# Performance work log

Measured on AMD Instinct MI355X. Metric: run time of the kernel, lower is better.

## Reference

```python
import jax, jax.numpy as jnp
import numpy as np

DIMS, K_SIZE, V_SIZE = 256, 64, 64
B, T = 4, 4096


def setup_inputs() -> dict:
    key = jax.random.key(0)
    k1, k2, k3, k4 = jax.random.split(key, 4)
    # glorot-uniform-style init for the projection weights
    def glorot(k, fan_in, fan_out):
        lim = jnp.sqrt(6.0 / (fan_in + fan_out))
        return jax.random.uniform(k, (fan_in, fan_out), jnp.float32, -lim, lim)
    return {
        "inputs": jax.random.normal(k1, (B, T, DIMS), jnp.float32),
        "key_w": glorot(k2, DIMS, K_SIZE),
        "query_w": glorot(k3, DIMS, K_SIZE),
        "value_w": glorot(k4, DIMS, V_SIZE),
    }


def reference(inputs, key_w, query_w, value_w):
    # QKV projections: [B,T,D] @ [D,k] -> [B,T,k]
    keys = jnp.einsum('btd,dk->btk', inputs, key_w)
    queries = jnp.einsum('btd,dk->btk', inputs, query_w)
    values = jnp.einsum('btd,dv->btv', inputs, value_w)
    # full causal score matrix [B,T,T] (faithful to explicit triu mask)
    logits = jnp.einsum('bqk,bsk->bqs', queries, keys)
    q_idx = jnp.arange(logits.shape[1])[:, None]
    s_idx = jnp.arange(logits.shape[2])[None, :]
    causal = s_idx <= q_idx  # lower-triangular incl. diagonal
    sqrt_k = jnp.sqrt(jnp.asarray(key_w.shape[1], jnp.float32))
    masked = jnp.where(causal[None], logits, -jnp.inf)
    probs = jax.nn.softmax(masked / sqrt_k, axis=2)
    read = jnp.einsum('bqs,bsv->bqv', probs, values)
    return jnp.concatenate([inputs, read], axis=-1)  # [B,T,D+V]
```

## Files before the change

### kernel.cpp

```cpp
#include <hip/hip_runtime.h>

#define DIMS 256
#define HK 64
#define NB 4
#define NT 4096
#define BT (NB * NT)
#define SMAX 8

typedef unsigned short u16;
typedef unsigned int u32;

using f32x4  = __attribute__((ext_vector_type(4))) float;
using bf16x8 = __attribute__((ext_vector_type(8))) short;
using u32x2  = __attribute__((ext_vector_type(2))) u32;

__device__ __forceinline__ u16 f2bf(float f) {
    u32 u = __float_as_uint(f);
    u = (u + 0x7FFFu + ((u >> 16) & 1u)) >> 16;
    return (u16)u;
}
__device__ __forceinline__ u32 pack2(float a, float b) {
    return (u32)f2bf(a) | ((u32)f2bf(b) << 16);
}
__device__ __forceinline__ float bf2f(short h) {
    return __uint_as_float(((u32)(u16)h) << 16);
}
__device__ __forceinline__ bf16x8 ldb8(const u16* p) {
    return *reinterpret_cast<const bf16x8*>(p);
}

__global__ __launch_bounds__(256) void prep_kernel(
    const float* __restrict__ x, const float* __restrict__ wk,
    const float* __restrict__ wq, const float* __restrict__ wv,
    float* __restrict__ out, u32* __restrict__ xb2, u16* __restrict__ Wt)
{
    const int stride = (int)(gridDim.x * blockDim.x);
    const int idx = (int)(blockIdx.x * blockDim.x + threadIdx.x);
    const f32x4* x4 = reinterpret_cast<const f32x4*>(x);
    f32x4* out4 = reinterpret_cast<f32x4*>(out);
    u32x2* xbv = reinterpret_cast<u32x2*>(xb2);

    for (int i = idx; i < BT * 64; i += stride) {
        f32x4 v = x4[i];
        out4[(size_t)(i >> 6) * 80 + (i & 63)] = v;
        u32x2 w;
        w.x = pack2(v[0], v[1]);
        w.y = pack2(v[2], v[3]);
        xbv[i] = w;
    }
    for (int i = idx; i < 12288; i += stride) {
        const int e0 = i * 4;
        const int m = e0 >> 14;
        const int r = e0 & 16383;
        const int col = r >> 8;
        const int k = r & 255;
        const float* w = (m == 0) ? wk : (m == 1) ? wq : wv;
        u32 w0 = pack2(w[(k + 0) * HK + col], w[(k + 1) * HK + col]);
        u32 w1 = pack2(w[(k + 2) * HK + col], w[(k + 3) * HK + col]);
        u32* p = reinterpret_cast<u32*>(Wt + e0);
        p[0] = w0; p[1] = w1;
    }
}

__global__ __launch_bounds__(64) void proj_kernel(
    const u16* __restrict__ xb, const u16* __restrict__ Wt,
    u16* __restrict__ Qb, u16* __restrict__ Kb, u16* __restrict__ Vt)
{
    const int l = (int)threadIdx.x;
    const int lo = l & 15;
    const int g = l >> 4;
    const int bid = (int)blockIdx.x;
    const int m = bid % 3;
    const int q0 = (bid / 3) * 16;

    bf16x8 a[8];
    const u16* xrow = xb + (size_t)(q0 + lo) * DIMS + g * 8;
    #pragma unroll
    for (int kf = 0; kf < 8; ++kf) a[kf] = ldb8(xrow + kf * 32);

    const u16* wb = Wt + m * (HK * DIMS);
    f32x4 acc[4];
    #pragma unroll
    for (int c = 0; c < 4; ++c) acc[c] = f32x4{0.f, 0.f, 0.f, 0.f};

    __builtin_amdgcn_s_setprio(1);
    #pragma unroll
    for (int c = 0; c < 4; ++c) {
        #pragma unroll
        for (int kf = 0; kf < 8; ++kf) {
            bf16x8 bf = ldb8(wb + (size_t)(16 * c + lo) * DIMS + kf * 32 + g * 8);
            acc[c] = __builtin_amdgcn_mfma_f32_16x16x32_bf16(a[kf], bf, acc[c], 0, 0, 0);
        }
    }
    __builtin_amdgcn_s_setprio(0);

    if (m == 2) {
        #pragma unroll
        for (int c = 0; c < 4; ++c)
            #pragma unroll
            for (int ii = 0; ii < 4; ++ii) {
                const int grow = q0 + 4 * g + ii;
                Vt[(size_t)((grow >> 12) * HK + 16 * c + lo) * NT + (grow & (NT - 1))] =
                    f2bf(acc[c][ii]);
            }
    } else {
        const float sc = (m == 1) ? 0.125f * 1.44269504f : 1.0f;
        u16* dst = (m == 1) ? Qb : Kb;
        #pragma unroll
        for (int c = 0; c < 4; ++c)
            #pragma unroll
            for (int ii = 0; ii < 4; ++ii)
                dst[(size_t)(q0 + 4 * g + ii) * HK + 16 * c + lo] = f2bf(acc[c][ii] * sc);
    }
}

template<bool MASK>
__device__ __forceinline__ void qk_tile(
    const u16* __restrict__ Kb_b, int s0, int colbase,
    const bf16x8 (&qf)[2][2], float (&pls)[2][4],
    u16 (&Pl)[32 * 72], int lo, int g, int q0)
{
    bf16x8 kk[2][2];
    #pragma unroll
    for (int kh = 0; kh < 2; ++kh)
        #pragma unroll
        for (int kf = 0; kf < 2; ++kf)
            kk[kh][kf] = ldb8(Kb_b + (size_t)(s0 + 16 * kh + lo) * HK + kf * 32 + g * 8);

    const f32x4 zz = f32x4{0.f, 0.f, 0.f, 0.f};
    f32x4 sv[2][2];
    __builtin_amdgcn_s_setprio(1);
    #pragma unroll
    for (int rh = 0; rh < 2; ++rh)
        #pragma unroll
        for (int kh = 0; kh < 2; ++kh) {
            sv[rh][kh] = __builtin_amdgcn_mfma_f32_16x16x32_bf16(qf[rh][0], kk[kh][0], zz, 0, 0, 0);
            sv[rh][kh] = __builtin_amdgcn_mfma_f32_16x16x32_bf16(qf[rh][1], kk[kh][1], sv[rh][kh], 0, 0, 0);
        }
    __builtin_amdgcn_s_setprio(0);

    #pragma unroll
    for (int rh = 0; rh < 2; ++rh)
        #pragma unroll
        for (int kh = 0; kh < 2; ++kh)
            #pragma unroll
            for (int ii = 0; ii < 4; ++ii) {
                float v = sv[rh][kh][ii];
                if (MASK) {
                    if (s0 + 16 * kh + lo > q0 + 16 * rh + 4 * g + ii) v = -1e30f;
                }
                const float p = __builtin_amdgcn_exp2f(v - 28.0f);
                pls[rh][ii] += p;
                Pl[(16 * rh + 4 * g + ii) * 72 + colbase + 16 * kh + lo] = f2bf(p);
            }
}

template<int NKF, bool MASK>
__device__ __forceinline__ void body(
    const u16* __restrict__ Kb_b, const u16* __restrict__ Vb, int s0,
    const bf16x8 (&qf)[2][2], float (&pls)[2][4], f32x4 (&o)[2][4],
    u16 (&Pl)[32 * 72], int lo, int g, int q0)
{
    bf16x8 vf[NKF][4];
    #pragma unroll
    for (int kf = 0; kf < NKF; ++kf)
        #pragma unroll
        for (int c = 0; c < 4; ++c)
            vf[kf][c] = ldb8(Vb + (size_t)(16 * c + lo) * NT + s0 + kf * 32 + g * 8);

    qk_tile<MASK>(Kb_b, s0, 0, qf, pls, Pl, lo, g, q0);
    if (NKF == 2) qk_tile<false>(Kb_b, s0 + 32, 32, qf, pls, Pl, lo, g, q0);

    bf16x8 pa[2][NKF];
    #pragma unroll
    for (int rh = 0; rh < 2; ++rh)
        #pragma unroll
        for (int kf = 0; kf < NKF; ++kf)
            pa[rh][kf] = *reinterpret_cast<const bf16x8*>(&Pl[(16 * rh + lo) * 72 + kf * 32 + g * 8]);

    __builtin_amdgcn_s_setprio(1);
    #pragma unroll
    for (int rh = 0; rh < 2; ++rh)
        #pragma unroll
        for (int c = 0; c < 4; ++c)
            #pragma unroll
            for (int kf = 0; kf < NKF; ++kf)
                o[rh][c] = __builtin_amdgcn_mfma_f32_16x16x32_bf16(pa[rh][kf], vf[kf][c], o[rh][c], 0, 0, 0);
    __builtin_amdgcn_s_setprio(0);
}

__global__ __launch_bounds__(64) void attn_kernel(
    const u16* __restrict__ Qb, const u16* __restrict__ Kb,
    const u16* __restrict__ Vt, u16* __restrict__ Opb, float* __restrict__ lp,
    const int S)
{
    __shared__ u16 Pl[32 * 72];
    const int l = (int)threadIdx.x;
    const int lo = l & 15;
    const int g = l >> 4;

    const int bid = (int)blockIdx.x;
    const int per = 4 * S;
    const int j = 127 - bid / per;
    const int r = bid % per;
    const int b = r / S;
    const int s = r % S;

    const int q0 = j * 32;
    const int nkv = j + 1;
    const int it0 = (s * nkv) / S;
    const int it1 = ((s + 1) * nkv) / S;

    const u16* Kb_b = Kb + (size_t)b * NT * HK;
    const u16* Vb = Vt + (size_t)b * HK * NT;

    bf16x8 qf[2][2];
    #pragma unroll
    for (int rh = 0; rh < 2; ++rh)
        #pragma unroll
        for (int kf = 0; kf < 2; ++kf)
            qf[rh][kf] = ldb8(Qb + (size_t)(b * NT + q0 + 16 * rh + lo) * HK + kf * 32 + g * 8);

    f32x4 o[2][4];
    float pls[2][4];
    #pragma unroll
    for (int rh = 0; rh < 2; ++rh)
        #pragma unroll
        for (int c = 0; c < 4; ++c) { o[rh][c] = f32x4{0.f, 0.f, 0.f, 0.f}; pls[rh][c] = 0.f; }

    int it = it0;
    const int itE = (s == S - 1) ? it1 - 1 : it1;
    for (; it + 1 < itE; it += 2)
        body<2, false>(Kb_b, Vb, it * 32, qf, pls, o, Pl, lo, g, q0);
    if (it < itE)
        body<1, false>(Kb_b, Vb, it * 32, qf, pls, o, Pl, lo, g, q0);
    if (s == S - 1)
        body<1, true>(Kb_b, Vb, (nkv - 1) * 32, qf, pls, o, Pl, lo, g, q0);

    const size_t rowbase = (size_t)s * BT + (size_t)b * NT + q0;
    #pragma unroll
    for (int rh = 0; rh < 2; ++rh) {
        #pragma unroll
        for (int c = 0; c < 4; ++c)
            #pragma unroll
            for (int ii = 0; ii < 4; ++ii)
                Opb[(rowbase + 16 * rh + 4 * g + ii) * HK + 16 * c + lo] = f2bf(o[rh][c][ii]);
        #pragma unroll
        for (int ii = 0; ii < 4; ++ii) {
            float sum = pls[rh][ii];
            sum += __shfl_xor(sum, 1);
            sum += __shfl_xor(sum, 2);
            sum += __shfl_xor(sum, 4);
            sum += __shfl_xor(sum, 8);
            if (lo == 0) lp[rowbase + 16 * rh + 4 * g + ii] = sum;
        }
    }
}

__global__ __launch_bounds__(256) void merge_kernel(
    const u16* __restrict__ Opb, const float* __restrict__ lp,
    float* __restrict__ out, const int S)
{
    const int idx = (int)(blockIdx.x * 256 + threadIdx.x);
    const int row = idx >> 3;
    const int c8 = (idx & 7) * 8;

    float li = 0.f;
    for (int s = 0; s < S; ++s) li += lp[(size_t)s * BT + row];

    float acc[8];
    #pragma unroll
    for (int k = 0; k < 8; ++k) acc[k] = 0.f;
    for (int s = 0; s < S; ++s) {
        bf16x8 v = ldb8(Opb + ((size_t)s * BT + row) * HK + c8);
        #pragma unroll
        for (int k = 0; k < 8; ++k) acc[k] += bf2f(v[k]);
    }
    const float inv = 1.0f / li;
    f32x4 r0 = f32x4{acc[0] * inv, acc[1] * inv, acc[2] * inv, acc[3] * inv};
    f32x4 r1 = f32x4{acc[4] * inv, acc[5] * inv, acc[6] * inv, acc[7] * inv};
    f32x4* dst = reinterpret_cast<f32x4*>(out + (size_t)row * 320 + 256 + c8);
    dst[0] = r0;
    dst[1] = r1;
}

extern "C" void kernel_launch(void* const* d_in, const int* in_sizes, int n_in,
                              void* d_out, int out_size, void* d_ws, size_t ws_size,
                              hipStream_t stream) {
    (void)in_sizes; (void)n_in; (void)out_size;
    const float* x  = (const float*)d_in[0];
    const float* wk = (const float*)d_in[1];
    const float* wq = (const float*)d_in[2];
    const float* wv = (const float*)d_in[3];
    float* out = (float*)d_out;

    char* ws = (char*)d_ws;
    u16* Qb  = (u16*)(ws);
    u16* Kb  = (u16*)(ws + ((size_t)2  << 20));
    u16* Vt  = (u16*)(ws + ((size_t)4  << 20));
    u32* xb2 = (u32*)(ws + ((size_t)6  << 20));
    u16* xb  = (u16*)xb2;
    u16* Wt  = (u16*)(ws + ((size_t)14 << 20));
    float* lp = (float*)(ws + ((size_t)15 << 20));
    u16* Opb = (u16*)(ws + ((size_t)16 << 20));

    int S = SMAX;
    while (S > 1 && ((size_t)16 << 20) + (size_t)S * BT * HK * 2 > ws_size) S >>= 1;

    prep_kernel<<<1024, 256, 0, stream>>>(x, wk, wq, wv, out, xb2, Wt);
    proj_kernel<<<3072, 64, 0, stream>>>(xb, Wt, Qb, Kb, Vt);
    attn_kernel<<<128 * 4 * S, 64, 0, stream>>>(Qb, Kb, Vt, Opb, lp, S);
    merge_kernel<<<512, 256, 0, stream>>>(Opb, lp, out, S);
}
```

Before: 75.09 us.

## Keep attention probabilities in registers via transposed QK MFMA and permlane swaps

Swaps the MFMA operand order so the score tile comes out transposed. Each lane then holds a key column slice that can be packed with v_cvt_pk_bf16_f32 and rearranged with permlane16/32 swaps straight into the A-operand layout for the PV MFMA. This removes the shared-memory round trip for P and the scalar software bf16 rounding. The -28 offset is folded into the MFMA accumulator init, and the row-sum reduction drops to two shuffles. It depends on gfx950-specific permlane instructions and on the swapped lane layout being correct, including the causal mask indices.

```diff
diff --git a/kernel.cpp b/kernel.cpp
--- a/kernel.cpp
+++ b/kernel.cpp
@@ -27,6 +27,11 @@
 }
 __device__ __forceinline__ bf16x8 ldb8(const u16* p) {
     return *reinterpret_cast<const bf16x8*>(p);
+}
+__device__ __forceinline__ u32 cvtpk(float a, float b) {
+    u32 r;
+    asm("v_cvt_pk_bf16_f32 %0, %1, %2" : "=v"(r) : "v"(a), "v"(b));
+    return r;
 }
 
 __global__ __launch_bounds__(256) void prep_kernel(
@@ -115,10 +120,10 @@
 }
 
 template<bool MASK>
-__device__ __forceinline__ void qk_tile(
-    const u16* __restrict__ Kb_b, int s0, int colbase,
-    const bf16x8 (&qf)[2][2], float (&pls)[2][4],
-    u16 (&Pl)[32 * 72], int lo, int g, int q0)
+__device__ __forceinline__ void qk32(
+    const u16* __restrict__ Kb_b, int s0, int q0,
+    const bf16x8 (&qf)[2][2], float (&pls)[2], bf16x8 (&pa)[2],
+    int lo, int g)
 {
     bf16x8 kk[2][2];
     #pragma unroll
@@ -127,66 +132,71 @@
         for (int kf = 0; kf < 2; ++kf)
             kk[kh][kf] = ldb8(Kb_b + (size_t)(s0 + 16 * kh + lo) * HK + kf * 32 + g * 8);
 
-    const f32x4 zz = f32x4{0.f, 0.f, 0.f, 0.f};
+    const f32x4 c28 = f32x4{-28.f, -28.f, -28.f, -28.f};
     f32x4 sv[2][2];
     __builtin_amdgcn_s_setprio(1);
     #pragma unroll
     for (int rh = 0; rh < 2; ++rh)
         #pragma unroll
         for (int kh = 0; kh < 2; ++kh) {
-            sv[rh][kh] = __builtin_amdgcn_mfma_f32_16x16x32_bf16(qf[rh][0], kk[kh][0], zz, 0, 0, 0);
-            sv[rh][kh] = __builtin_amdgcn_mfma_f32_16x16x32_bf16(qf[rh][1], kk[kh][1], sv[rh][kh], 0, 0, 0);
+            sv[rh][kh] = __builtin_amdgcn_mfma_f32_16x16x32_bf16(kk[kh][0], qf[rh][0], c28, 0, 0, 0);
+            sv[rh][kh] = __builtin_amdgcn_mfma_f32_16x16x32_bf16(kk[kh][1], qf[rh][1], sv[rh][kh], 0, 0, 0);
         }
     __builtin_amdgcn_s_setprio(0);
 
     #pragma unroll
-    for (int rh = 0; rh < 2; ++rh)
-        #pragma unroll
-        for (int kh = 0; kh < 2; ++kh)
-            #pragma unroll
-            for (int ii = 0; ii < 4; ++ii) {
-                float v = sv[rh][kh][ii];
-                if (MASK) {
-                    if (s0 + 16 * kh + lo > q0 + 16 * rh + 4 * g + ii) v = -1e30f;
-                }
-                const float p = __builtin_amdgcn_exp2f(v - 28.0f);
-                pls[rh][ii] += p;
-                Pl[(16 * rh + 4 * g + ii) * 72 + colbase + 16 * kh + lo] = f2bf(p);
+    for (int rh = 0; rh < 2; ++rh) {
+        float p0[4], p1[4];
+        #pragma unroll
+        for (int ii = 0; ii < 4; ++ii) {
+            float v0 = sv[rh][0][ii];
+            float v1 = sv[rh][1][ii];
+            if (MASK) {
+                const int qr = q0 + 16 * rh + lo;
+                if (s0 + 4 * g + ii > qr)      v0 = -1e30f;
+                if (s0 + 16 + 4 * g + ii > qr) v1 = -1e30f;
             }
-}
-
-template<int NKF, bool MASK>
+            p0[ii] = __builtin_amdgcn_exp2f(v0);
+            p1[ii] = __builtin_amdgcn_exp2f(v1);
+            pls[rh] += p0[ii] + p1[ii];
+        }
+        u32 a0 = cvtpk(p0[0], p0[1]), a1 = cvtpk(p0[2], p0[3]);
+        u32 b0 = cvtpk(p1[0], p1[1]), b1 = cvtpk(p1[2], p1[3]);
+        asm("v_permlane32_swap_b32 %0, %1" : "+v"(a0), "+v"(b0));
+        asm("v_permlane16_swap_b32 %0, %1" : "+v"(a0), "+v"(b0));
+        asm("v_permlane32_swap_b32 %0, %1" : "+v"(a1), "+v"(b1));
+        asm("v_permlane16_swap_b32 %0, %1" : "+v"(a1), "+v"(b1));
+        union { u32 w[4]; bf16x8 v; } u;
+        u.w[0] = a0; u.w[1] = a1; u.w[2] = b0; u.w[3] = b1;
+        pa[rh] = u.v;
+    }
+}
+
+template<int NK, bool MASK>
 __device__ __forceinline__ void body(
     const u16* __restrict__ Kb_b, const u16* __restrict__ Vb, int s0,
-    const bf16x8 (&qf)[2][2], float (&pls)[2][4], f32x4 (&o)[2][4],
-    u16 (&Pl)[32 * 72], int lo, int g, int q0)
-{
-    bf16x8 vf[NKF][4];
-    #pragma unroll
-    for (int kf = 0; kf < NKF; ++kf)
+    const bf16x8 (&qf)[2][2], float (&pls)[2], f32x4 (&o)[2][4],
+    int lo, int g, int q0)
+{
+    bf16x8 vf[NK][4];
+    #pragma unroll
+    for (int kf = 0; kf < NK; ++kf)
         #pragma unroll
         for (int c = 0; c < 4; ++c)
             vf[kf][c] = ldb8(Vb + (size_t)(16 * c + lo) * NT + s0 + kf * 32 + g * 8);
 
-    qk_tile<MASK>(Kb_b, s0, 0, qf, pls, Pl, lo, g, q0);
-    if (NKF == 2) qk_tile<false>(Kb_b, s0 + 32, 32, qf, pls, Pl, lo, g, q0);
-
-    bf16x8 pa[2][NKF];
-    #pragma unroll
-    for (int rh = 0; rh < 2; ++rh)
-        #pragma unroll
-        for (int kf = 0; kf < NKF; ++kf)
-            pa[rh][kf] = *reinterpret_cast<const bf16x8*>(&Pl[(16 * rh + lo) * 72 + kf * 32 + g * 8]);
-
-    __builtin_amdgcn_s_setprio(1);
-    #pragma unroll
-    for (int rh = 0; rh < 2; ++rh)
-        #pragma unroll
-        for (int c = 0; c < 4; ++c)
+    #pragma unroll
+    for (int t = 0; t < NK; ++t) {
+        bf16x8 pa[2];
+        qk32<MASK>(Kb_b, s0 + t * 32, q0, qf, pls, pa, lo, g);
+        __builtin_amdgcn_s_setprio(1);
+        #pragma unroll
+        for (int rh = 0; rh < 2; ++rh)
             #pragma unroll
-            for (int kf = 0; kf < NKF; ++kf)
-                o[rh][c] = __builtin_amdgcn_mfma_f32_16x16x32_bf16(pa[rh][kf], vf[kf][c], o[rh][c], 0, 0, 0);
-    __builtin_amdgcn_s_setprio(0);
+            for (int c = 0; c < 4; ++c)
+                o[rh][c] = __builtin_amdgcn_mfma_f32_16x16x32_bf16(pa[rh], vf[t][c], o[rh][c], 0, 0, 0);
+        __builtin_amdgcn_s_setprio(0);
+    }
 }
 
 __global__ __launch_bounds__(64) void attn_kernel(
@@ -194,7 +204,6 @@
     const u16* __restrict__ Vt, u16* __restrict__ Opb, float* __restrict__ lp,
     const int S)
 {
-    __shared__ u16 Pl[32 * 72];
     const int l = (int)threadIdx.x;
     const int lo = l & 15;
     const int g = l >> 4;
@@ -222,20 +231,20 @@
             qf[rh][kf] = ldb8(Qb + (size_t)(b * NT + q0 + 16 * rh + lo) * HK + kf * 32 + g * 8);
 
     f32x4 o[2][4];
-    float pls[2][4];
+    float pls[2] = {0.f, 0.f};
     #pragma unroll
     for (int rh = 0; rh < 2; ++rh)
         #pragma unroll
-        for (int c = 0; c < 4; ++c) { o[rh][c] = f32x4{0.f, 0.f, 0.f, 0.f}; pls[rh][c] = 0.f; }
+        for (int c = 0; c < 4; ++c) o[rh][c] = f32x4{0.f, 0.f, 0.f, 0.f};
 
     int it = it0;
     const int itE = (s == S - 1) ? it1 - 1 : it1;
     for (; it + 1 < itE; it += 2)
-        body<2, false>(Kb_b, Vb, it * 32, qf, pls, o, Pl, lo, g, q0);
+        body<2, false>(Kb_b, Vb, it * 32, qf, pls, o, lo, g, q0);
     if (it < itE)
-        body<1, false>(Kb_b, Vb, it * 32, qf, pls, o, Pl, lo, g, q0);
+        body<1, false>(Kb_b, Vb, it * 32, qf, pls, o, lo, g, q0);
     if (s == S - 1)
-        body<1, true>(Kb_b, Vb, (nkv - 1) * 32, qf, pls, o, Pl, lo, g, q0);
+        body<1, true>(Kb_b, Vb, (nkv - 1) * 32, qf, pls, o, lo, g, q0);
 
     const size_t rowbase = (size_t)s * BT + (size_t)b * NT + q0;
     #pragma unroll
@@ -245,15 +254,10 @@
             #pragma unroll
             for (int ii = 0; ii < 4; ++ii)
                 Opb[(rowbase + 16 * rh + 4 * g + ii) * HK + 16 * c + lo] = f2bf(o[rh][c][ii]);
-        #pragma unroll
-        for (int ii = 0; ii < 4; ++ii) {
-            float sum = pls[rh][ii];
-            sum += __shfl_xor(sum, 1);
-            sum += __shfl_xor(sum, 2);
-            sum += __shfl_xor(sum, 4);
-            sum += __shfl_xor(sum, 8);
-            if (lo == 0) lp[rowbase + 16 * rh + 4 * g + ii] = sum;
-        }
+        float sum = pls[rh];
+        sum += __shfl_xor(sum, 16);
+        sum += __shfl_xor(sum, 32);
+        if (l < 16) lp[rowbase + 16 * rh + lo] = sum;
     }
 }
 
```

Result: no change. 76.05 us (+1.3%).
